# Optimization experiments

Hardware: AMD Instinct MI355X
Metric: run time of the kernel (lower is better)

Reference implementation:

```python
import jax, jax.numpy as jnp
import numpy as np

N_NODES = 100000
N_EDGES = 600000
N_GRAPHS = 256
HID = 128
IN_DIM = 7
POCKET_DIM = 28
BN_EPS = 1e-5


def setup_inputs() -> dict:
    key = jax.random.key(0)
    ks = jax.random.split(key, 24)
    d = {}
    d['x'] = jax.random.normal(ks[0], (N_NODES, IN_DIM), dtype=jnp.float32)
    d['edge_index'] = jax.random.randint(ks[1], (2, N_EDGES), 0, N_NODES, dtype=jnp.int32)
    d['batch'] = jnp.sort(jax.random.randint(ks[2], (N_NODES,), 0, N_GRAPHS, dtype=jnp.int32))
    d['pocket'] = jax.random.normal(ks[3], (POCKET_DIM,), dtype=jnp.float32)
    # GCN layer weights (PyG GCNConv: lin then normalized aggregation, bias after)
    def glorot(k, shape):
        lim = np.sqrt(6.0 / (shape[0] + shape[1]))
        return jax.random.uniform(k, shape, jnp.float32, -lim, lim)
    d['W0'] = glorot(ks[4], (IN_DIM, HID)); d['b0'] = jnp.zeros((HID,), jnp.float32)
    d['W1'] = glorot(ks[5], (HID, HID)); d['b1'] = jnp.zeros((HID,), jnp.float32)
    d['W2'] = glorot(ks[6], (HID, HID)); d['b2'] = jnp.zeros((HID,), jnp.float32)
    # BatchNorm (eval mode) params for 3 layers
    d['bn_gamma'] = jax.random.uniform(ks[7], (3, HID), jnp.float32, 0.5, 1.5)
    d['bn_beta'] = 0.1 * jax.random.normal(ks[8], (3, HID), dtype=jnp.float32)
    d['bn_mean'] = 0.1 * jax.random.normal(ks[9], (3, HID), dtype=jnp.float32)
    d['bn_var'] = jax.random.uniform(ks[10], (3, HID), jnp.float32, 0.5, 1.5)
    # pocket MLP: 28 -> 64 -> 64
    d['pw1'] = glorot(ks[11], (POCKET_DIM, 64)); d['pb1'] = jnp.zeros((64,), jnp.float32)
    d['pw2'] = glorot(ks[12], (64, 64)); d['pb2'] = jnp.zeros((64,), jnp.float32)
    # classifier: 192 -> 96 -> 1
    d['cw1'] = glorot(ks[13], (HID + 64, 96)); d['cb1'] = jnp.zeros((96,), jnp.float32)
    d['cw2'] = glorot(ks[14], (96, 1)); d['cb2'] = jnp.zeros((1,), jnp.float32)
    return d


def reference(x, edge_index, batch, pocket, W0, b0, W1, b1, W2, b2,
              bn_gamma, bn_beta, bn_mean, bn_var,
              pw1, pb1, pw2, pb2, cw1, cb1, cw2, cb2):
    src, dst = edge_index[0], edge_index[1]
    n = x.shape[0]
    # degree with self-loops (GCNConv default add_self_loops=True)
    deg = jax.ops.segment_sum(jnp.ones((src.shape[0],), x.dtype), dst, num_segments=n) + 1.0
    dinv = jax.lax.rsqrt(deg)                      # [N]
    norm = dinv[src] * dinv[dst]                   # [E] edge normalization
    self_norm = (dinv * dinv)[:, None]             # [N,1] self-loop norm

    h = x
    for i, (W, b) in enumerate(((W0, b0), (W1, b1), (W2, b2))):
        hl = h @ W                                  # [N,HID]
        agg = jax.ops.segment_sum(hl[src] * norm[:, None], dst, num_segments=n)
        agg = agg + hl * self_norm + b
        # BatchNorm1d in eval mode with running stats
        bn = (agg - bn_mean[i]) * (bn_gamma[i] * jax.lax.rsqrt(bn_var[i] + BN_EPS)) + bn_beta[i]
        h = jax.nn.relu(bn)                         # dropout is identity in eval

    # global mean pool over graphs
    sums = jax.ops.segment_sum(h, batch, num_segments=N_GRAPHS)          # [B,HID]
    cnts = jax.ops.segment_sum(jnp.ones((n,), h.dtype), batch, num_segments=N_GRAPHS)
    lig = sums / jnp.maximum(cnts, 1.0)[:, None]

    # pocket MLP, broadcast to batch
    p = jax.nn.relu(pocket @ pw1 + pb1) @ pw2 + pb2                      # [64]
    pe = jnp.broadcast_to(p[None, :], (N_GRAPHS, 64))

    emb = jnp.concatenate([lig, pe], axis=1)                             # [B,192]
    logits = (jax.nn.relu(emb @ cw1 + cb1) @ cw2 + cb2)[:, 0]            # [B]
    return logits
```

## Files before the change

### kernel.cpp

```cpp
#include <hip/hip_runtime.h>

#define NN 100000
#define NE 600000
#define NG 256
#define HID 128
#define BN_EPS 1e-5f

#define SCAN_TILE 1024
#define NTILES ((NN + SCAN_TILE - 1) / SCAN_TILE)

typedef __attribute__((ext_vector_type(8))) short short8;
typedef __attribute__((ext_vector_type(4))) float float4v;

__device__ __forceinline__ unsigned short f2bf_rn(float f) {
    unsigned u = __float_as_uint(f);
    unsigned r = u + 0x7FFFu + ((u >> 16) & 1u);
    return (unsigned short)(r >> 16);
}
__device__ __forceinline__ float bf2f(unsigned short h) {
    return __uint_as_float((unsigned)h << 16);
}
__device__ __forceinline__ float4 us4tof4(ushort4 u) {
    return make_float4(bf2f(u.x), bf2f(u.y), bf2f(u.z), bf2f(u.w));
}


__global__ __launch_bounds__(256) void hist_kernel(const int* __restrict__ dst, int* __restrict__ cnt) {
    int e = blockIdx.x * blockDim.x + threadIdx.x;
    if (e < NE) atomicAdd(&cnt[dst[e]], 1);
}


__global__ __launch_bounds__(256) void scan_a(const int* __restrict__ cnt, int* __restrict__ rs,
                                              int* __restrict__ tsum, float* __restrict__ dinv) {
    __shared__ int s[256];
    int t = threadIdx.x;
    int base = blockIdx.x * SCAN_TILE;
    int idx = base + t * 4;
    int v0 = (idx + 0 < NN) ? cnt[idx + 0] : 0;
    int v1 = (idx + 1 < NN) ? cnt[idx + 1] : 0;
    int v2 = (idx + 2 < NN) ? cnt[idx + 2] : 0;
    int v3 = (idx + 3 < NN) ? cnt[idx + 3] : 0;
    if (idx + 0 < NN) dinv[idx + 0] = rsqrtf((float)v0 + 1.0f);
    if (idx + 1 < NN) dinv[idx + 1] = rsqrtf((float)v1 + 1.0f);
    if (idx + 2 < NN) dinv[idx + 2] = rsqrtf((float)v2 + 1.0f);
    if (idx + 3 < NN) dinv[idx + 3] = rsqrtf((float)v3 + 1.0f);
    int local = v0 + v1 + v2 + v3;
    s[t] = local;
    __syncthreads();
    for (int off = 1; off < 256; off <<= 1) {
        int x = (t >= off) ? s[t - off] : 0;
        __syncthreads();
        s[t] += x;
        __syncthreads();
    }
    int pre = s[t] - local;
    if (t == 255) tsum[blockIdx.x] = s[255];
    if (idx + 0 < NN) rs[idx + 0] = pre; pre += v0;
    if (idx + 1 < NN) rs[idx + 1] = pre; pre += v1;
    if (idx + 2 < NN) rs[idx + 2] = pre; pre += v2;
    if (idx + 3 < NN) rs[idx + 3] = pre;
}

__global__ __launch_bounds__(128) void scan_b(int* __restrict__ tsum) {
    __shared__ int s[128];
    int t = threadIdx.x;
    int v = (t < NTILES) ? tsum[t] : 0;
    s[t] = v;
    __syncthreads();
    for (int off = 1; off < 128; off <<= 1) {
        int x = (t >= off) ? s[t - off] : 0;
        __syncthreads();
        s[t] += x;
        __syncthreads();
    }
    if (t < NTILES) tsum[t] = s[t] - v;
}

__global__ __launch_bounds__(256) void scan_c(int* __restrict__ rs, const int* __restrict__ tsum,
                                              int* __restrict__ cursor) {
    int t = threadIdx.x;
    int base = blockIdx.x * SCAN_TILE;
    int off = tsum[blockIdx.x];
    for (int k = 0; k < 4; k++) {
        int idx = base + t * 4 + k;
        if (idx < NN) {
            int v = rs[idx] + off;
            rs[idx] = v;
            cursor[idx] = v;
        }
    }
    if (blockIdx.x == 0 && t == 0) rs[NN] = NE;
}


__global__ __launch_bounds__(256) void bucket_kernel(const int* __restrict__ src, const int* __restrict__ dst,
                                                     const float* __restrict__ dinv,
                                                     int* __restrict__ cursor,
                                                     int* __restrict__ esrc, float* __restrict__ ewt) {
    int e = blockIdx.x * blockDim.x + threadIdx.x;
    if (e < NE) {
        int s = src[e], d = dst[e];
        int pos = atomicAdd(&cursor[d], 1);
        esrc[pos] = s;
        ewt[pos] = dinv[s] * dinv[d];
    }
}


__global__ __launch_bounds__(256) void prep_kernel(const float* __restrict__ W1, const float* __restrict__ W2,
                                                   unsigned short* __restrict__ w1hi, unsigned short* __restrict__ w1lo,
                                                   unsigned short* __restrict__ w2hi, unsigned short* __restrict__ w2lo,
                                                   const float* __restrict__ pocket,
                                                   const float* __restrict__ pw1, const float* __restrict__ pb1,
                                                   const float* __restrict__ pw2, const float* __restrict__ pb2,
                                                   float* __restrict__ pv) {
    if (blockIdx.x < 64) {
        int t = blockIdx.x * 256 + threadIdx.x;
        int k = t >> 7, n = t & 127;
        int to = n * HID + k;
        float v1 = W1[t];
        unsigned short h1 = f2bf_rn(v1);
        w1hi[to] = h1;
        w1lo[to] = f2bf_rn(v1 - bf2f(h1));
        float v2 = W2[t];
        unsigned short h2 = f2bf_rn(v2);
        w2hi[to] = h2;
        w2lo[to] = f2bf_rn(v2 - bf2f(h2));
    } else {
        __shared__ float t1[64];
        int j = threadIdx.x;
        if (j < 64) {
            float acc = pb1[j];
            for (int k = 0; k < 28; k++) acc = fmaf(pocket[k], pw1[k * 64 + j], acc);
            t1[j] = fmaxf(acc, 0.f);
        }
        __syncthreads();
        if (j < 64) {
            float acc2 = pb2[j];
            for (int k = 0; k < 64; k++) acc2 = fmaf(t1[k], pw2[k * 64 + j], acc2);
            pv[j] = acc2;
        }
    }
}


__global__ __launch_bounds__(256) void xagg_kernel(const float* __restrict__ x,
                                                   const int* __restrict__ rs,
                                                   const int* __restrict__ esrc,
                                                   const float* __restrict__ ewt,
                                                   const float* __restrict__ dinv,
                                                   float* __restrict__ xa) {
    int t = blockIdx.x * blockDim.x + threadIdx.x;
    int f = t & 7;
    int n = t >> 3;
    if (n >= NN) return;
    float acc = 0.f;
    if (f < 7) {
        float di = dinv[n];
        acc = x[n * 7 + f] * di * di;
        int e0 = rs[n], e1 = rs[n + 1];
        int e = e0;
        for (; e + 1 < e1; e += 2) {
            int s0 = esrc[e], s1 = esrc[e + 1];
            float w0 = ewt[e], w1 = ewt[e + 1];
            float a0 = x[s0 * 7 + f];
            float a1 = x[s1 * 7 + f];
            acc = fmaf(a0, w0, acc);
            acc = fmaf(a1, w1, acc);
        }
        if (e < e1) acc = fmaf(x[esrc[e] * 7 + f], ewt[e], acc);
    }
    xa[n * 8 + f] = acc;
}


__global__ __launch_bounds__(256) void l0_transform(const float* __restrict__ xa,
                                                    const float* __restrict__ W,
                                                    const float* __restrict__ b,
                                                    const float* __restrict__ gamma,
                                                    const float* __restrict__ beta,
                                                    const float* __restrict__ mean,
                                                    const float* __restrict__ var,
                                                    unsigned short* __restrict__ ohi) {
    int c4 = threadIdx.x & 31;
    int r  = threadIdx.x >> 5;
    float w[7][4];
#pragma unroll
    for (int k = 0; k < 7; k++)
#pragma unroll
        for (int i = 0; i < 4; i++) w[k][i] = W[k * HID + c4 * 4 + i];
    float4 bb = ((const float4*)b)[c4];
    float4 ga = ((const float4*)gamma)[c4];
    float4 be = ((const float4*)beta)[c4];
    float4 me = ((const float4*)mean)[c4];
    float4 va = ((const float4*)var)[c4];
    float4 sc;
    sc.x = ga.x * rsqrtf(va.x + BN_EPS);
    sc.y = ga.y * rsqrtf(va.y + BN_EPS);
    sc.z = ga.z * rsqrtf(va.z + BN_EPS);
    sc.w = ga.w * rsqrtf(va.w + BN_EPS);
    __shared__ float s[8][8];
    for (int n0 = blockIdx.x * 8; n0 < NN; n0 += gridDim.x * 8) {
        __syncthreads();
        if (threadIdx.x < 64) s[threadIdx.x >> 3][threadIdx.x & 7] = xa[n0 * 8 + threadIdx.x];
        __syncthreads();
        float o0 = bb.x, o1 = bb.y, o2 = bb.z, o3 = bb.w;
#pragma unroll
        for (int k = 0; k < 7; k++) {
            float xv = s[r][k];
            o0 = fmaf(xv, w[k][0], o0);
            o1 = fmaf(xv, w[k][1], o1);
            o2 = fmaf(xv, w[k][2], o2);
            o3 = fmaf(xv, w[k][3], o3);
        }
        ushort4 hi4;
        hi4.x = f2bf_rn(fmaxf(fmaf(o0 - me.x, sc.x, be.x), 0.f));
        hi4.y = f2bf_rn(fmaxf(fmaf(o1 - me.y, sc.y, be.y), 0.f));
        hi4.z = f2bf_rn(fmaxf(fmaf(o2 - me.z, sc.z, be.z), 0.f));
        hi4.w = f2bf_rn(fmaxf(fmaf(o3 - me.w, sc.w, be.w), 0.f));
        *(ushort4*)(ohi + (size_t)(n0 + r) * HID + c4 * 4) = hi4;
    }
}


__global__ __launch_bounds__(256) void mm_mfma(const unsigned short* __restrict__ A,
                                               const unsigned short* __restrict__ Whi,
                                               const unsigned short* __restrict__ Wlo,
                                               unsigned short* __restrict__ out) {
    int wave = threadIdx.x >> 6;
    int lane = threadIdx.x & 63;
    int mrow = lane & 15;
    int quad = lane >> 4;
    int m0 = blockIdx.x * 32;
    int n0 = wave * 32;

    short8 bh[2][4], bl[2][4];
#pragma unroll
    for (int ct = 0; ct < 2; ct++) {
#pragma unroll
        for (int kc = 0; kc < 4; kc++) {
            size_t off = (size_t)(n0 + ct * 16 + mrow) * HID + kc * 32 + quad * 8;
            bh[ct][kc] = *(const short8*)(Whi + off);
            bl[ct][kc] = *(const short8*)(Wlo + off);
        }
    }

    float4v acc[2][2];
#pragma unroll
    for (int rt = 0; rt < 2; rt++)
#pragma unroll
        for (int ct = 0; ct < 2; ct++) {
            acc[rt][ct].x = 0.f; acc[rt][ct].y = 0.f;
            acc[rt][ct].z = 0.f; acc[rt][ct].w = 0.f;
        }

#pragma unroll
    for (int kc = 0; kc < 4; kc++) {
#pragma unroll
        for (int rt = 0; rt < 2; rt++) {
            size_t aoff = (size_t)(m0 + rt * 16 + mrow) * HID + kc * 32 + quad * 8;
            short8 ah = *(const short8*)(A + aoff);
#pragma unroll
            for (int ct = 0; ct < 2; ct++) {
                acc[rt][ct] = __builtin_amdgcn_mfma_f32_16x16x32_bf16(ah, bh[ct][kc], acc[rt][ct], 0, 0, 0);
                acc[rt][ct] = __builtin_amdgcn_mfma_f32_16x16x32_bf16(ah, bl[ct][kc], acc[rt][ct], 0, 0, 0);
            }
        }
    }

#pragma unroll
    for (int rt = 0; rt < 2; rt++) {
#pragma unroll
        for (int ct = 0; ct < 2; ct++) {
            int col = n0 + ct * 16 + mrow;
#pragma unroll
            for (int r = 0; r < 4; r++) {
                int row = m0 + rt * 16 + quad * 4 + r;
                out[(size_t)row * HID + col] = f2bf_rn(acc[rt][ct][r]);
            }
        }
    }
}


template <bool BF16OUT>
__global__ __launch_bounds__(256) void gather_bn_t(const unsigned short* __restrict__ hl,
                                                   const int* __restrict__ rs,
                                                   const int* __restrict__ esrc,
                                                   const float* __restrict__ ewt,
                                                   const float* __restrict__ dinv,
                                                   const float* __restrict__ b,
                                                   const float* __restrict__ gamma,
                                                   const float* __restrict__ beta,
                                                   const float* __restrict__ mean,
                                                   const float* __restrict__ var,
                                                   float* __restrict__ outf,
                                                   unsigned short* __restrict__ ohi) {
    int t = blockIdx.x * blockDim.x + threadIdx.x;
    int lane = t & 31;
    int n = t >> 5;
    if (n >= NN) return;
    const ushort4* hl4 = (const ushort4*)hl;
    float di = dinv[n];
    float4 self = us4tof4(hl4[(size_t)n * 32 + lane]);
    float4 bb = ((const float4*)b)[lane];
    float dsq = di * di;
    float4 acc;
    acc.x = fmaf(self.x, dsq, bb.x);
    acc.y = fmaf(self.y, dsq, bb.y);
    acc.z = fmaf(self.z, dsq, bb.z);
    acc.w = fmaf(self.w, dsq, bb.w);
    int e0 = rs[n], e1 = rs[n + 1];
    int e = e0;
    for (; e + 1 < e1; e += 2) {
        int s0 = esrc[e], s1 = esrc[e + 1];
        float w0 = ewt[e], w1 = ewt[e + 1];
        float4 v0 = us4tof4(hl4[(size_t)s0 * 32 + lane]);
        float4 v1 = us4tof4(hl4[(size_t)s1 * 32 + lane]);
        acc.x = fmaf(v0.x, w0, acc.x); acc.y = fmaf(v0.y, w0, acc.y);
        acc.z = fmaf(v0.z, w0, acc.z); acc.w = fmaf(v0.w, w0, acc.w);
        acc.x = fmaf(v1.x, w1, acc.x); acc.y = fmaf(v1.y, w1, acc.y);
        acc.z = fmaf(v1.z, w1, acc.z); acc.w = fmaf(v1.w, w1, acc.w);
    }
    if (e < e1) {
        int s0 = esrc[e];
        float w0 = ewt[e];
        float4 v0 = us4tof4(hl4[(size_t)s0 * 32 + lane]);
        acc.x = fmaf(v0.x, w0, acc.x); acc.y = fmaf(v0.y, w0, acc.y);
        acc.z = fmaf(v0.z, w0, acc.z); acc.w = fmaf(v0.w, w0, acc.w);
    }
    float4 ga = ((const float4*)gamma)[lane];
    float4 be = ((const float4*)beta)[lane];
    float4 me = ((const float4*)mean)[lane];
    float4 va = ((const float4*)var)[lane];
    float4 o;
    o.x = fmaxf(fmaf(acc.x - me.x, ga.x * rsqrtf(va.x + BN_EPS), be.x), 0.f);
    o.y = fmaxf(fmaf(acc.y - me.y, ga.y * rsqrtf(va.y + BN_EPS), be.y), 0.f);
    o.z = fmaxf(fmaf(acc.z - me.z, ga.z * rsqrtf(va.z + BN_EPS), be.z), 0.f);
    o.w = fmaxf(fmaf(acc.w - me.w, ga.w * rsqrtf(va.w + BN_EPS), be.w), 0.f);
    if (BF16OUT) {
        ushort4 hi4;
        hi4.x = f2bf_rn(o.x);
        hi4.y = f2bf_rn(o.y);
        hi4.z = f2bf_rn(o.z);
        hi4.w = f2bf_rn(o.w);
        ((ushort4*)ohi)[(size_t)n * 32 + lane] = hi4;
    } else {
        ((float4*)outf)[(size_t)n * 32 + lane] = o;
    }
}


__global__ __launch_bounds__(1024) void poolcls_kernel(const float* __restrict__ h,
                                                       const int* __restrict__ batch,
                                                       const float* __restrict__ pv,
                                                       const float* __restrict__ cw1,
                                                       const float* __restrict__ cb1,
                                                       const float* __restrict__ cw2,
                                                       const float* __restrict__ cb2,
                                                       float* __restrict__ out) {
    int g = blockIdx.x;
    int lane = threadIdx.x & 31;
    int row = threadIdx.x >> 5;
    __shared__ int se[2];
    __shared__ float emb[192];
    __shared__ float hid[96];
    if (threadIdx.x < 2) {
        int target = g + threadIdx.x;
        int lo = 0, hi = NN;
        while (lo < hi) {
            int mid = (lo + hi) >> 1;
            if (batch[mid] < target) lo = mid + 1; else hi = mid;
        }
        se[threadIdx.x] = lo;
    }
    if (threadIdx.x < 64) emb[128 + threadIdx.x] = pv[threadIdx.x];
    __syncthreads();
    int start = se[0], end = se[1];
    const float4* h4 = (const float4*)h;
    float4 acc = make_float4(0.f, 0.f, 0.f, 0.f);
    for (int n = start + row; n < end; n += 32) {
        float4 v = h4[(size_t)n * 32 + lane];
        acc.x += v.x; acc.y += v.y; acc.z += v.z; acc.w += v.w;
    }
    __shared__ float4 part[32][32];
    part[row][lane] = acc;
    __syncthreads();
#pragma unroll
    for (int off = 16; off >= 1; off >>= 1) {
        if (row < off) {
            float4 a = part[row][lane];
            float4 c = part[row + off][lane];
            a.x += c.x; a.y += c.y; a.z += c.z; a.w += c.w;
            part[row][lane] = a;
        }
        __syncthreads();
    }
    if (row == 0) {
        float inv = 1.0f / fmaxf((float)(end - start), 1.0f);
        float4 a = part[0][lane];
        a.x *= inv; a.y *= inv; a.z *= inv; a.w *= inv;
        ((float4*)emb)[lane] = a;
    }
    __syncthreads();
    int j = threadIdx.x;
    if (j < 96) {
        float a = cb1[j];
        for (int k = 0; k < 192; k++) a = fmaf(emb[k], cw1[k * 96 + j], a);
        hid[j] = fmaxf(a, 0.f) * cw2[j];
    }
    __syncthreads();
    if (j == 0) {
        float s = cb2[0];
        for (int k = 0; k < 96; k++) s += hid[k];
        out[g] = s;
    }
}

extern "C" void kernel_launch(void* const* d_in, const int* in_sizes, int n_in,
                              void* d_out, int out_size, void* d_ws, size_t ws_size,
                              hipStream_t stream) {
    const float* x        = (const float*)d_in[0];
    const int*   eidx     = (const int*)d_in[1];
    const int*   batch    = (const int*)d_in[2];
    const float* pocket   = (const float*)d_in[3];
    const float* W0 = (const float*)d_in[4];
    const float* b0 = (const float*)d_in[5];
    const float* W1 = (const float*)d_in[6];
    const float* b1 = (const float*)d_in[7];
    const float* W2 = (const float*)d_in[8];
    const float* b2 = (const float*)d_in[9];
    const float* bn_gamma = (const float*)d_in[10];
    const float* bn_beta  = (const float*)d_in[11];
    const float* bn_mean  = (const float*)d_in[12];
    const float* bn_var   = (const float*)d_in[13];
    const float* pw1 = (const float*)d_in[14]; const float* pb1 = (const float*)d_in[15];
    const float* pw2 = (const float*)d_in[16]; const float* pb2 = (const float*)d_in[17];
    const float* cw1 = (const float*)d_in[18]; const float* cb1 = (const float*)d_in[19];
    const float* cw2 = (const float*)d_in[20]; const float* cb2 = (const float*)d_in[21];
    float* out = (float*)d_out;

    float* ws   = (float*)d_ws;
    float* dinv = ws;
    int*   cnt  = (int*)(ws + NN);
    int*   rs   = cnt + NN;
    int*   tsum = rs + NN + 1;
    int*   esrc = tsum + 128;
    float* ewt  = (float*)(esrc + NE);
    float* xa   = ewt + NE;
    unsigned short* w1hi = (unsigned short*)(xa + (size_t)NN * 8);
    unsigned short* w1lo = w1hi + HID * HID;
    unsigned short* w2hi = w1lo + HID * HID;
    unsigned short* w2lo = w2hi + HID * HID;
    size_t head = (size_t)NN * 2 + (NN + 1) + 128 + (size_t)NE * 2 + (size_t)NN * 8
                + (4 * HID * HID) / 2;
    head = (head + 3) & ~(size_t)3;
    float* R1   = ws + head;
    unsigned short* A = (unsigned short*)R1;
    float* Cf   = R1;
    unsigned short* B = (unsigned short*)(R1 + (size_t)NN * HID);
    float* pv   = R1 + (size_t)NN * HID + (size_t)NN * HID / 2;

    const int* srcp = eidx;
    const int* dstp = eidx + NE;

    hipMemsetAsync(cnt, 0, NN * sizeof(int), stream);
    hist_kernel<<<(NE + 255) / 256, 256, 0, stream>>>(dstp, cnt);
    scan_a<<<NTILES, 256, 0, stream>>>(cnt, rs, tsum, dinv);
    scan_b<<<1, 128, 0, stream>>>(tsum);
    scan_c<<<NTILES, 256, 0, stream>>>(rs, tsum, cnt);
    bucket_kernel<<<(NE + 255) / 256, 256, 0, stream>>>(srcp, dstp, dinv, cnt, esrc, ewt);
    prep_kernel<<<65, 256, 0, stream>>>(W1, W2, w1hi, w1lo, w2hi, w2lo,
                                        pocket, pw1, pb1, pw2, pb2, pv);

    xagg_kernel<<<(NN * 8 + 255) / 256, 256, 0, stream>>>(x, rs, esrc, ewt, dinv, xa);
    l0_transform<<<2048, 256, 0, stream>>>(xa, W0, b0,
                                           bn_gamma + 0 * HID, bn_beta + 0 * HID,
                                           bn_mean + 0 * HID, bn_var + 0 * HID, A);

    const int MM_BLOCKS = NN / 32;

    mm_mfma<<<MM_BLOCKS, 256, 0, stream>>>(A, w1hi, w1lo, B);
    gather_bn_t<true><<<(NN * 32 + 255) / 256, 256, 0, stream>>>(
        B, rs, esrc, ewt, dinv, b1,
        bn_gamma + 1 * HID, bn_beta + 1 * HID, bn_mean + 1 * HID, bn_var + 1 * HID,
        nullptr, A);
    mm_mfma<<<MM_BLOCKS, 256, 0, stream>>>(A, w2hi, w2lo, B);
    gather_bn_t<false><<<(NN * 32 + 255) / 256, 256, 0, stream>>>(
        B, rs, esrc, ewt, dinv, b2,
        bn_gamma + 2 * HID, bn_beta + 2 * HID, bn_mean + 2 * HID, bn_var + 2 * HID,
        Cf, nullptr);

    poolcls_kernel<<<NG, 1024, 0, stream>>>(Cf, batch, pv, cw1, cb1, cw2, cb2, out);
}
```

Baseline: 380.5 us.

## Persistent prefetching MFMA GEMM and 16-byte-per-lane gather with 4-edge unroll

The GEMM kernel becomes persistent over 1024 blocks. Each block loads its weight fragments once and prefetches the next tile's A fragments while computing the current one, which amortises the weight loads and overlaps global loads with MFMA work. The gather/BN kernel now uses 16 lanes per node, each loading 16 bytes (8 bf16) per neighbor, with the edge loop unrolled by 4. This gives wider memory transactions and more outstanding gathers per thread, at the cost of more registers and fewer threads per node.

Result: faster. 342.6 us (-10.0%).

```diff
diff --git a/kernel.cpp b/kernel.cpp
--- a/kernel.cpp
+++ b/kernel.cpp
@@ -8,6 +8,7 @@
 
 #define SCAN_TILE 1024
 #define NTILES ((NN + SCAN_TILE - 1) / SCAN_TILE)
+#define MM_TILES (NN / 32)
 
 typedef __attribute__((ext_vector_type(8))) short short8;
 typedef __attribute__((ext_vector_type(4))) float float4v;
@@ -20,8 +21,11 @@
 __device__ __forceinline__ float bf2f(unsigned short h) {
     return __uint_as_float((unsigned)h << 16);
 }
-__device__ __forceinline__ float4 us4tof4(ushort4 u) {
-    return make_float4(bf2f(u.x), bf2f(u.y), bf2f(u.z), bf2f(u.w));
+__device__ __forceinline__ void unpack8(uint4 u, float* f) {
+    f[0] = __uint_as_float(u.x << 16); f[1] = __uint_as_float(u.x & 0xFFFF0000u);
+    f[2] = __uint_as_float(u.y << 16); f[3] = __uint_as_float(u.y & 0xFFFF0000u);
+    f[4] = __uint_as_float(u.z << 16); f[5] = __uint_as_float(u.z & 0xFFFF0000u);
+    f[6] = __uint_as_float(u.w << 16); f[7] = __uint_as_float(u.w & 0xFFFF0000u);
 }
 
 
@@ -232,7 +236,6 @@
     int lane = threadIdx.x & 63;
     int mrow = lane & 15;
     int quad = lane >> 4;
-    int m0 = blockIdx.x * 32;
     int n0 = wave * 32;
 
     short8 bh[2][4], bl[2][4];
@@ -246,40 +249,66 @@
         }
     }
 
-    float4v acc[2][2];
+    int tile = blockIdx.x;
+    if (tile >= MM_TILES) return;
+
+    short8 ah[2][4];
 #pragma unroll
     for (int rt = 0; rt < 2; rt++)
 #pragma unroll
-        for (int ct = 0; ct < 2; ct++) {
-            acc[rt][ct].x = 0.f; acc[rt][ct].y = 0.f;
-            acc[rt][ct].z = 0.f; acc[rt][ct].w = 0.f;
-        }
-
-#pragma unroll
-    for (int kc = 0; kc < 4; kc++) {
-#pragma unroll
-        for (int rt = 0; rt < 2; rt++) {
-            size_t aoff = (size_t)(m0 + rt * 16 + mrow) * HID + kc * 32 + quad * 8;
-            short8 ah = *(const short8*)(A + aoff);
+        for (int kc = 0; kc < 4; kc++)
+            ah[rt][kc] = *(const short8*)(A + (size_t)(tile * 32 + rt * 16 + mrow) * HID + kc * 32 + quad * 8);
+
+    for (;;) {
+        int nt = tile + gridDim.x;
+        bool has_next = nt < MM_TILES;
+        short8 an[2][4];
+        if (has_next) {
+#pragma unroll
+            for (int rt = 0; rt < 2; rt++)
+#pragma unroll
+                for (int kc = 0; kc < 4; kc++)
+                    an[rt][kc] = *(const short8*)(A + (size_t)(nt * 32 + rt * 16 + mrow) * HID + kc * 32 + quad * 8);
+        }
+
+        float4v acc[2][2];
+#pragma unroll
+        for (int rt = 0; rt < 2; rt++)
 #pragma unroll
             for (int ct = 0; ct < 2; ct++) {
-                acc[rt][ct] = __builtin_amdgcn_mfma_f32_16x16x32_bf16(ah, bh[ct][kc], acc[rt][ct], 0, 0, 0);
-                acc[rt][ct] = __builtin_amdgcn_mfma_f32_16x16x32_bf16(ah, bl[ct][kc], acc[rt][ct], 0, 0, 0);
+                acc[rt][ct].x = 0.f; acc[rt][ct].y = 0.f;
+                acc[rt][ct].z = 0.f; acc[rt][ct].w = 0.f;
             }
-        }
-    }
-
-#pragma unroll
-    for (int rt = 0; rt < 2; rt++) {
-#pragma unroll
-        for (int ct = 0; ct < 2; ct++) {
-            int col = n0 + ct * 16 + mrow;
-#pragma unroll
-            for (int r = 0; r < 4; r++) {
-                int row = m0 + rt * 16 + quad * 4 + r;
-                out[(size_t)row * HID + col] = f2bf_rn(acc[rt][ct][r]);
+
+#pragma unroll
+        for (int kc = 0; kc < 4; kc++)
+#pragma unroll
+            for (int rt = 0; rt < 2; rt++)
+#pragma unroll
+                for (int ct = 0; ct < 2; ct++) {
+                    acc[rt][ct] = __builtin_amdgcn_mfma_f32_16x16x32_bf16(ah[rt][kc], bh[ct][kc], acc[rt][ct], 0, 0, 0);
+                    acc[rt][ct] = __builtin_amdgcn_mfma_f32_16x16x32_bf16(ah[rt][kc], bl[ct][kc], acc[rt][ct], 0, 0, 0);
+                }
+
+        int m0 = tile * 32;
+#pragma unroll
+        for (int rt = 0; rt < 2; rt++)
+#pragma unroll
+            for (int ct = 0; ct < 2; ct++) {
+                int col = n0 + ct * 16 + mrow;
+#pragma unroll
+                for (int r = 0; r < 4; r++) {
+                    int row = m0 + rt * 16 + quad * 4 + r;
+                    out[(size_t)row * HID + col] = f2bf_rn(acc[rt][ct][r]);
+                }
             }
-        }
+
+        if (!has_next) break;
+#pragma unroll
+        for (int rt = 0; rt < 2; rt++)
+#pragma unroll
+            for (int kc = 0; kc < 4; kc++) ah[rt][kc] = an[rt][kc];
+        tile = nt;
     }
 }
 
@@ -298,56 +327,80 @@
                                                    float* __restrict__ outf,
                                                    unsigned short* __restrict__ ohi) {
     int t = blockIdx.x * blockDim.x + threadIdx.x;
-    int lane = t & 31;
-    int n = t >> 5;
+    int lane = t & 15;
+    int n = t >> 4;
     if (n >= NN) return;
-    const ushort4* hl4 = (const ushort4*)hl;
+    const uint4* hlv = (const uint4*)hl;
     float di = dinv[n];
-    float4 self = us4tof4(hl4[(size_t)n * 32 + lane]);
-    float4 bb = ((const float4*)b)[lane];
     float dsq = di * di;
-    float4 acc;
-    acc.x = fmaf(self.x, dsq, bb.x);
-    acc.y = fmaf(self.y, dsq, bb.y);
-    acc.z = fmaf(self.z, dsq, bb.z);
-    acc.w = fmaf(self.w, dsq, bb.w);
+
+    float acc[8], v[8];
+    {
+        uint4 sv = hlv[(size_t)n * 16 + lane];
+        unpack8(sv, v);
+        float4 bA = ((const float4*)b)[lane * 2];
+        float4 bB = ((const float4*)b)[lane * 2 + 1];
+        acc[0] = fmaf(v[0], dsq, bA.x); acc[1] = fmaf(v[1], dsq, bA.y);
+        acc[2] = fmaf(v[2], dsq, bA.z); acc[3] = fmaf(v[3], dsq, bA.w);
+        acc[4] = fmaf(v[4], dsq, bB.x); acc[5] = fmaf(v[5], dsq, bB.y);
+        acc[6] = fmaf(v[6], dsq, bB.z); acc[7] = fmaf(v[7], dsq, bB.w);
+    }
+
     int e0 = rs[n], e1 = rs[n + 1];
     int e = e0;
-    for (; e + 1 < e1; e += 2) {
-        int s0 = esrc[e], s1 = esrc[e + 1];
-        float w0 = ewt[e], w1 = ewt[e + 1];
-        float4 v0 = us4tof4(hl4[(size_t)s0 * 32 + lane]);
-        float4 v1 = us4tof4(hl4[(size_t)s1 * 32 + lane]);
-        acc.x = fmaf(v0.x, w0, acc.x); acc.y = fmaf(v0.y, w0, acc.y);
-        acc.z = fmaf(v0.z, w0, acc.z); acc.w = fmaf(v0.w, w0, acc.w);
-        acc.x = fmaf(v1.x, w1, acc.x); acc.y = fmaf(v1.y, w1, acc.y);
-        acc.z = fmaf(v1.z, w1, acc.z); acc.w = fmaf(v1.w, w1, acc.w);
-    }
-    if (e < e1) {
+    for (; e + 3 < e1; e += 4) {
+        int s0 = esrc[e], s1 = esrc[e + 1], s2 = esrc[e + 2], s3 = esrc[e + 3];
+        float w0 = ewt[e], w1 = ewt[e + 1], w2 = ewt[e + 2], w3 = ewt[e + 3];
+        uint4 u0 = hlv[(size_t)s0 * 16 + lane];
+        uint4 u1 = hlv[(size_t)s1 * 16 + lane];
+        uint4 u2 = hlv[(size_t)s2 * 16 + lane];
+        uint4 u3 = hlv[(size_t)s3 * 16 + lane];
+        unpack8(u0, v);
+#pragma unroll
+        for (int i = 0; i < 8; i++) acc[i] = fmaf(v[i], w0, acc[i]);
+        unpack8(u1, v);
+#pragma unroll
+        for (int i = 0; i < 8; i++) acc[i] = fmaf(v[i], w1, acc[i]);
+        unpack8(u2, v);
+#pragma unroll
+        for (int i = 0; i < 8; i++) acc[i] = fmaf(v[i], w2, acc[i]);
+        unpack8(u3, v);
+#pragma unroll
+        for (int i = 0; i < 8; i++) acc[i] = fmaf(v[i], w3, acc[i]);
+    }
+    for (; e < e1; e++) {
         int s0 = esrc[e];
         float w0 = ewt[e];
-        float4 v0 = us4tof4(hl4[(size_t)s0 * 32 + lane]);
-        acc.x = fmaf(v0.x, w0, acc.x); acc.y = fmaf(v0.y, w0, acc.y);
-        acc.z = fmaf(v0.z, w0, acc.z); acc.w = fmaf(v0.w, w0, acc.w);
-    }
-    float4 ga = ((const float4*)gamma)[lane];
-    float4 be = ((const float4*)beta)[lane];
-    float4 me = ((const float4*)mean)[lane];
-    float4 va = ((const float4*)var)[lane];
-    float4 o;
-    o.x = fmaxf(fmaf(acc.x - me.x, ga.x * rsqrtf(va.x + BN_EPS), be.x), 0.f);
-    o.y = fmaxf(fmaf(acc.y - me.y, ga.y * rsqrtf(va.y + BN_EPS), be.y), 0.f);
-    o.z = fmaxf(fmaf(acc.z - me.z, ga.z * rsqrtf(va.z + BN_EPS), be.z), 0.f);
-    o.w = fmaxf(fmaf(acc.w - me.w, ga.w * rsqrtf(va.w + BN_EPS), be.w), 0.f);
+        uint4 u0 = hlv[(size_t)s0 * 16 + lane];
+        unpack8(u0, v);
+#pragma unroll
+        for (int i = 0; i < 8; i++) acc[i] = fmaf(v[i], w0, acc[i]);
+    }
+
+    float4 gA = ((const float4*)gamma)[lane * 2], gB = ((const float4*)gamma)[lane * 2 + 1];
+    float4 eA = ((const float4*)beta)[lane * 2],  eB = ((const float4*)beta)[lane * 2 + 1];
+    float4 mA = ((const float4*)mean)[lane * 2],  mB = ((const float4*)mean)[lane * 2 + 1];
+    float4 vA = ((const float4*)var)[lane * 2],   vB = ((const float4*)var)[lane * 2 + 1];
+    float o[8];
+    o[0] = fmaxf(fmaf(acc[0] - mA.x, gA.x * rsqrtf(vA.x + BN_EPS), eA.x), 0.f);
+    o[1] = fmaxf(fmaf(acc[1] - mA.y, gA.y * rsqrtf(vA.y + BN_EPS), eA.y), 0.f);
+    o[2] = fmaxf(fmaf(acc[2] - mA.z, gA.z * rsqrtf(vA.z + BN_EPS), eA.z), 0.f);
+    o[3] = fmaxf(fmaf(acc[3] - mA.w, gA.w * rsqrtf(vA.w + BN_EPS), eA.w), 0.f);
+    o[4] = fmaxf(fmaf(acc[4] - mB.x, gB.x * rsqrtf(vB.x + BN_EPS), eB.x), 0.f);
+    o[5] = fmaxf(fmaf(acc[5] - mB.y, gB.y * rsqrtf(vB.y + BN_EPS), eB.y), 0.f);
+    o[6] = fmaxf(fmaf(acc[6] - mB.z, gB.z * rsqrtf(vB.z + BN_EPS), eB.z), 0.f);
+    o[7] = fmaxf(fmaf(acc[7] - mB.w, gB.w * rsqrtf(vB.w + BN_EPS), eB.w), 0.f);
+
     if (BF16OUT) {
-        ushort4 hi4;
-        hi4.x = f2bf_rn(o.x);
-        hi4.y = f2bf_rn(o.y);
-        hi4.z = f2bf_rn(o.z);
-        hi4.w = f2bf_rn(o.w);
-        ((ushort4*)ohi)[(size_t)n * 32 + lane] = hi4;
+        uint4 p;
+        p.x = (unsigned)f2bf_rn(o[0]) | ((unsigned)f2bf_rn(o[1]) << 16);
+        p.y = (unsigned)f2bf_rn(o[2]) | ((unsigned)f2bf_rn(o[3]) << 16);
+        p.z = (unsigned)f2bf_rn(o[4]) | ((unsigned)f2bf_rn(o[5]) << 16);
+        p.w = (unsigned)f2bf_rn(o[6]) | ((unsigned)f2bf_rn(o[7]) << 16);
+        ((uint4*)ohi)[(size_t)n * 16 + lane] = p;
     } else {
-        ((float4*)outf)[(size_t)n * 32 + lane] = o;
+        ((float4*)outf)[(size_t)n * 32 + lane * 2]     = make_float4(o[0], o[1], o[2], o[3]);
+        ((float4*)outf)[(size_t)n * 32 + lane * 2 + 1] = make_float4(o[4], o[5], o[6], o[7]);
     }
 }
 
@@ -479,15 +532,16 @@
                                            bn_gamma + 0 * HID, bn_beta + 0 * HID,
                                            bn_mean + 0 * HID, bn_var + 0 * HID, A);
 
-    const int MM_BLOCKS = NN / 32;
+    const int MM_BLOCKS = 1024;
+    const int GA_BLOCKS = (NN * 16 + 255) / 256;
 
     mm_mfma<<<MM_BLOCKS, 256, 0, stream>>>(A, w1hi, w1lo, B);
-    gather_bn_t<true><<<(NN * 32 + 255) / 256, 256, 0, stream>>>(
+    gather_bn_t<true><<<GA_BLOCKS, 256, 0, stream>>>(
         B, rs, esrc, ewt, dinv, b1,
         bn_gamma + 1 * HID, bn_beta + 1 * HID, bn_mean + 1 * HID, bn_var + 1 * HID,
         nullptr, A);
     mm_mfma<<<MM_BLOCKS, 256, 0, stream>>>(A, w2hi, w2lo, B);
-    gather_bn_t<false><<<(NN * 32 + 255) / 256, 256, 0, stream>>>(
+    gather_bn_t<false><<<GA_BLOCKS, 256, 0, stream>>>(
         B, rs, esrc, ewt, dinv, b2,
         bn_gamma + 2 * HID, bn_beta + 2 * HID, bn_mean + 2 * HID, bn_var + 2 * HID,
         Cf, nullptr);
```
